# Optimization experiments

Hardware: AMD Instinct MI355X
Metric: run time of the kernel (lower is better)

The kernel has to match this reference:

```python
import jax, jax.numpy as jnp
import numpy as np

N_NODES = 5000
N_STRUCT = 50
PER = N_NODES // N_STRUCT
K = 24
N_EDGES = N_NODES * K
MAX_EDGES = 32
D = 128
HEADS = 4
L = 2
M = 1
NSP = 4
ALL_SPECIES = np.array([1, 6, 7, 8])
R_CUT, R_TRANS = 5.0, 3.0
SPECIES_TABLE = jnp.full((9,), -1, dtype=jnp.int32).at[jnp.asarray(ALL_SPECIES)].set(jnp.arange(NSP, dtype=jnp.int32))

def _ln(x, w, b):
    m = jnp.mean(x, axis=-1, keepdims=True)
    v = jnp.var(x, axis=-1, keepdims=True)
    return (x - m) * jax.lax.rsqrt(v + 1e-5) * w + b

def _block(x, mask, Wq, Wk, Wv, Wo, l1w, l1b, l2w, l2b, W1, b1, W2, b2):
    n, t, d = x.shape
    dh = d // HEADS
    h = _ln(x, l1w, l1b)
    q = (h @ Wq).reshape(n, t, HEADS, dh)
    k = (h @ Wk).reshape(n, t, HEADS, dh)
    v = (h @ Wv).reshape(n, t, HEADS, dh)
    scores = jnp.einsum('nthd,nshd->nhts', q, k) * (1.0 / np.sqrt(dh))
    p = jax.nn.softmax(scores, axis=-1) * mask[:, None, None, :]  # cutoff-weighted keys
    x = x + jnp.einsum('nhts,nshd->nthd', p, v).reshape(n, t, d) @ Wo
    h2 = _ln(x, l2w, l2b)
    return x + jax.nn.gelu(h2 @ W1 + b1) @ W2 + b2

def _transformer(x, mask, params):
    for i in range(L):
        x = _block(x, mask, *(a[i] for a in params))
    return x

def _graph_indices(centers, neighbors):
    e_ids = jnp.arange(N_EDGES, dtype=jnp.int32)
    counts = jnp.zeros((N_NODES,), jnp.int32).at[centers].add(1)
    start = jnp.cumsum(counts) - counts
    slot = e_ids - start[centers]  # centers sorted by construction
    nef_idx = jnp.zeros((N_NODES, MAX_EDGES), jnp.int32).at[centers, slot].set(e_ids)
    nef_mask = jnp.arange(MAX_EDGES, dtype=jnp.int32)[None, :] < counts[:, None]
    keys = centers * N_NODES + neighbors
    order = jnp.argsort(keys)
    corr = order[jnp.searchsorted(keys[order], neighbors * N_NODES + centers)]
    return nef_idx, slot, nef_mask, corr

def _cutoff(r):
    x = (r - R_TRANS) / (R_CUT - R_TRANS)
    smooth = 0.5 * (1.0 + jnp.cos(jnp.pi * x))
    return jnp.where(r < R_TRANS, 1.0, jnp.where(r >= R_CUT, 0.0, smooth))

def _forward(positions, cells, cell_shifts, enc_Wcart, enc_emb_center, enc_emb_neigh, enc_Wcomp, t_Wq, t_Wk, t_Wv, t_Wo, t_ln1w, t_ln1b, t_ln2w, t_ln2b, t_W1, t_b1, t_W2, t_b2, g_contr, g_Wq, g_Wk, g_Wv, g_Wo, g_ln1w, g_ln1b, g_ln2w, g_ln2b, g_W1, g_b1, g_W2, g_b2, readout_W, composition_weights, numbers, centers, neighbors):
    seg = jnp.repeat(jnp.arange(N_STRUCT, dtype=jnp.int32), PER)  # sorted structure ids
    ev = positions[neighbors] - positions[centers] + jnp.einsum('ia,iab->ib', cell_shifts, cells[seg[centers]])
    radial = _cutoff(jnp.sqrt(jnp.sum(ev * ev, axis=-1)))
    elem = SPECIES_TABLE[numbers]
    nef_idx, slot, nef_mask, corr = _graph_indices(centers, neighbors)
    radial_nef = jnp.where(nef_mask, radial[nef_idx], 0.0)
    feats = jnp.concatenate([ev[nef_idx] @ enc_Wcart, enc_emb_center[elem[centers][nef_idx]], enc_emb_neigh[elem[neighbors][nef_idx]]], axis=-1) @ enc_Wcomp
    tparams = (t_Wq, t_Wk, t_Wv, t_Wo, t_ln1w, t_ln1b, t_ln2w, t_ln2b, t_W1, t_b1, t_W2, t_b2)
    feats = _transformer(feats, radial_nef, tparams)
    gparams = (g_Wq, g_Wk, g_Wv, g_Wo, g_ln1w, g_ln1b, g_ln2w, g_ln2b, g_W1, g_b1, g_W2, g_b2)
    for m in range(M):
        new = feats[centers, slot]  # nef -> edge list
        new = jnp.concatenate([new, new[corr]], axis=-1) @ g_contr[m]
        new = _transformer(new[nef_idx], radial_nef, tuple(a[m] for a in gparams))
        feats = feats + new
    ee = (feats @ readout_W)[..., 0] * radial_nef  # [N, MAX_EDGES]
    struct_e = jax.ops.segment_sum(jnp.sum(ee, axis=1), seg, num_segments=N_STRUCT, indices_are_sorted=True)
    comp = jax.ops.segment_sum(jax.nn.one_hot(elem, NSP, dtype=jnp.float32), seg, num_segments=N_STRUCT, indices_are_sorted=True)
    return struct_e + comp @ composition_weights

def setup_inputs():
    key = jax.random.key(0)
    ks = jax.random.split(key, 24)
    deltas = np.concatenate([np.arange(1, K // 2 + 1), -np.arange(1, K // 2 + 1)])
    nb_local = (np.arange(PER)[:, None] + deltas[None, :]) % PER  # symmetric circulant graph per structure
    neighbors = (nb_local[None, :, :] + (np.arange(N_STRUCT) * PER)[:, None, None]).reshape(-1)
    centers = np.repeat(np.arange(N_NODES), K)
    def w(i, shape, s=0.05):
        return (jax.random.normal(ks[i], shape) * s).astype(jnp.float32)
    return {
        'positions': jax.random.normal(ks[0], (N_NODES, 3), dtype=jnp.float32) * 2.0,
        'cells': jnp.tile(jnp.eye(3, dtype=jnp.float32) * 20.0, (N_STRUCT, 1, 1)),
        'cell_shifts': jnp.zeros((N_EDGES, 3), dtype=jnp.float32),
        'enc_Wcart': w(2, (3, D), 0.5),
        'enc_emb_center': w(3, (NSP, D), 1.0),
        'enc_emb_neigh': w(4, (NSP, D), 1.0),
        'enc_Wcomp': w(5, (3 * D, D)),
        't_Wq': w(6, (L, D, D)), 't_Wk': w(7, (L, D, D)), 't_Wv': w(8, (L, D, D)), 't_Wo': w(9, (L, D, D)),
        't_ln1w': jnp.ones((L, D), jnp.float32), 't_ln1b': jnp.zeros((L, D), jnp.float32),
        't_ln2w': jnp.ones((L, D), jnp.float32), 't_ln2b': jnp.zeros((L, D), jnp.float32),
        't_W1': w(10, (L, D, 4 * D)), 't_b1': jnp.zeros((L, 4 * D), jnp.float32),
        't_W2': w(11, (L, 4 * D, D)), 't_b2': jnp.zeros((L, D), jnp.float32),
        'g_contr': w(12, (M, 2 * D, D)),
        'g_Wq': w(13, (M, L, D, D)), 'g_Wk': w(14, (M, L, D, D)), 'g_Wv': w(15, (M, L, D, D)), 'g_Wo': w(16, (M, L, D, D)),
        'g_ln1w': jnp.ones((M, L, D), jnp.float32), 'g_ln1b': jnp.zeros((M, L, D), jnp.float32),
        'g_ln2w': jnp.ones((M, L, D), jnp.float32), 'g_ln2b': jnp.zeros((M, L, D), jnp.float32),
        'g_W1': w(17, (M, L, D, 4 * D)), 'g_b1': jnp.zeros((M, L, 4 * D), jnp.float32),
        'g_W2': w(18, (M, L, 4 * D, D)), 'g_b2': jnp.zeros((M, L, D), jnp.float32),
        'readout_W': w(19, (D, 1)),
        'composition_weights': w(20, (NSP,), 1.0),
        'numbers': jnp.asarray(ALL_SPECIES, dtype=jnp.int32)[jax.random.randint(ks[1], (N_NODES,), 0, NSP)],
        'centers': jnp.asarray(centers, dtype=jnp.int32),
        'neighbors': jnp.asarray(neighbors, dtype=jnp.int32),
    }

def reference(positions, cells, cell_shifts, enc_Wcart, enc_emb_center, enc_emb_neigh, enc_Wcomp, t_Wq, t_Wk, t_Wv, t_Wo, t_ln1w, t_ln1b, t_ln2w, t_ln2b, t_W1, t_b1, t_W2, t_b2, g_contr, g_Wq, g_Wk, g_Wv, g_Wo, g_ln1w, g_ln1b, g_ln2w, g_ln2b, g_W1, g_b1, g_W2, g_b2, readout_W, composition_weights, numbers, centers, neighbors):
    return _forward(positions, cells, cell_shifts, enc_Wcart, enc_emb_center, enc_emb_neigh, enc_Wcomp, t_Wq, t_Wk, t_Wv, t_Wo, t_ln1w, t_ln1b, t_ln2w, t_ln2b, t_W1, t_b1, t_W2, t_b2, g_contr, g_Wq, g_Wk, g_Wv, g_Wo, g_ln1w, g_ln1b, g_ln2w, g_ln2b, g_W1, g_b1, g_W2, g_b2, readout_W, composition_weights, numbers, centers, neighbors)
```

## Files before the change

kernel.cpp:

```cpp
#include <hip/hip_runtime.h>
#include <hip/hip_bf16.h>
#include <math.h>

#define N_NODES 5000
#define N_STRUCT 50
#define PER 100
#define K_NB 24
#define N_EDGES (N_NODES*K_NB)
#define TMAX 32
#define D 128
#define FF 512
#define NTOK (N_NODES*TMAX)

typedef short bf16x8 __attribute__((ext_vector_type(8)));
typedef float f32x4  __attribute__((ext_vector_type(4)));
#define MFMA_B16(a,b,c) __builtin_amdgcn_mfma_f32_16x16x32_bf16(a,b,c,0,0,0)

__device__ __forceinline__ short f2bf(float x){
    return (short)((__float_as_uint(x) + 0x8000u) >> 16);
}
__device__ __forceinline__ short f2bf_rn(float x){
    unsigned u = __float_as_uint(x);
    return (short)((u + 0x7FFFu + ((u>>16)&1u)) >> 16);
}

__device__ __forceinline__ float gelu_f(float x){
    float arg = x * fmaf(x*x, -0.07135481627f, -1.5957691216057308f);
    return x * __builtin_amdgcn_rcpf(1.f + __expf(arg));
}

__device__ __forceinline__ float cutoff_f(float r){
    if (r < 3.f) return 1.f;
    if (r >= 5.f) return 0.f;
    float x = (r-3.f)*0.5f;
    return 0.5f*(1.f + cosf(3.14159265358979323846f * x));
}

__global__ void k_setup(const float* tWq, const float* tWk, const float* tWv, const float* tWo,
                        const float* tW1, const float* tW2, const float* gWq, const float* gWk,
                        const float* gWv, const float* gWo, const float* gW1, const float* gW2,
                        const float* gct, short* __restrict__ WT,
                        const float* __restrict__ pos, const float* __restrict__ cells,
                        const float* __restrict__ shifts, const int* __restrict__ centers,
                        const int* __restrict__ neighbors, float* __restrict__ EV,
                        float* __restrict__ RAD, int* __restrict__ CORR,
                        const int* __restrict__ numbers, int* __restrict__ ELEM,
                        const float* __restrict__ Wcart, const float* __restrict__ embc,
                        const float* __restrict__ embn, const float* __restrict__ Wcomp,
                        float* __restrict__ W3, float* __restrict__ ECn, float* __restrict__ ENn,
                        float* __restrict__ out){
    int b = blockIdx.x, tid = threadIdx.x;
    if (b < 3200){
        const int  sel[25]  = {0,0,1,1,2,2,3,3,4,4,5,5,6,6,7,7,8,8,9,9,10,10,11,11,12};
        const int  lin[25]  = {7,7,7,7,7,7,7,7,7,7,9,9,7,7,7,7,7,7,7,7,7,7,9,9,8};
        const int  lout[25] = {7,7,7,7,7,7,7,7,9,9,7,7,7,7,7,7,7,7,7,7,9,9,7,7,7};
        const int  soff[25] = {0,16384,0,16384,0,16384,0,16384,0,65536,0,65536,
                               0,16384,0,16384,0,16384,0,16384,0,65536,0,65536,0};
        const int  doff[25] = {0,16384,32768,49152,65536,81920,98304,114688,
                               131072,196608,262144,327680,
                               393216,409600,425984,442368,458752,475136,491520,507904,
                               524288,589824,655360,720896,786432};
        int gid = b*256 + tid;
        int r = 0, base = 0;
        while (true){
            int sz = 1 << (lin[r]+lout[r]);
            if (gid < base + sz) break;
            base += sz; r++;
        }
        int d = gid - base;
        int j = d >> lin[r], i = d & ((1<<lin[r])-1);
        const float* src;
        switch (sel[r]){
            case 0: src=tWq; break; case 1: src=tWk; break; case 2: src=tWv; break; case 3: src=tWo; break;
            case 4: src=tW1; break; case 5: src=tW2; break;
            case 6: src=gWq; break; case 7: src=gWk; break; case 8: src=gWv; break; case 9: src=gWo; break;
            case 10: src=gW1; break; case 11: src=gW2; break; default: src=gct; break;
        }
        float v = src[soff[r] + (i<<lout[r]) + j];
        if (sel[r] == 0 || sel[r] == 6) v *= 0.17677669529663689f;
        WT[doff[r] + d] = f2bf_rn(v);
    } else if (b < 3669){
        int e = (b-3200)*256 + tid;
        if (e >= N_EDGES) return;
        int c = centers[e], nb = neighbors[e];
        int st = c / PER;
        const float* cell = cells + st*9;
        float s0 = shifts[e*3+0], s1 = shifts[e*3+1], s2 = shifts[e*3+2];
        float ex = pos[nb*3+0]-pos[c*3+0] + s0*cell[0]+s1*cell[3]+s2*cell[6];
        float ey = pos[nb*3+1]-pos[c*3+1] + s0*cell[1]+s1*cell[4]+s2*cell[7];
        float ez = pos[nb*3+2]-pos[c*3+2] + s0*cell[2]+s1*cell[5]+s2*cell[8];
        EV[e*3+0] = ex; EV[e*3+1] = ey; EV[e*3+2] = ez;
        RAD[e] = cutoff_f(sqrtf(ex*ex+ey*ey+ez*ez));
        int base2 = nb*K_NB, corr = base2;
        for (int k2 = 0; k2 < K_NB; k2++){
            if (neighbors[base2+k2] == c){ corr = base2+k2; break; }
        }
        CORR[e] = corr;
    } else if (b < 3689){
        int i = (b-3669)*256 + tid;
        if (i < N_NODES){
            int z = numbers[i];
            ELEM[i] = (z==1)?0:(z==6)?1:(z==7)?2:(z==8)?3:-1;
        }
    } else if (b == 3689){
        if (tid >= 128) return;
        int j = tid;
        for (int a = 0; a < 3; a++){
            float s = 0;
            for (int i = 0; i < 128; i++) s += Wcart[a*128+i]*Wcomp[i*128+j];
            W3[a*128+j] = s;
        }
        for (int sp = 0; sp < 4; sp++){
            float s1 = 0, s2 = 0;
            for (int i = 0; i < 128; i++){
                s1 += embc[sp*128+i]*Wcomp[(128+i)*128+j];
                s2 += embn[sp*128+i]*Wcomp[(256+i)*128+j];
            }
            ECn[sp*128+j] = s1; ENn[sp*128+j] = s2;
        }
    } else {
        if (tid < N_STRUCT) out[tid] = 0.f;
    }
}

__global__ __launch_bounds__(256) void k_encode(const float* __restrict__ EV,
                         const float* __restrict__ RAD,
                         const int* __restrict__ centers, const int* __restrict__ neighbors,
                         const int* __restrict__ ELEM, const float* __restrict__ W3,
                         const float* __restrict__ ECn, const float* __restrict__ ENn,
                         float* __restrict__ X, float* __restrict__ RADN){
    int n = blockIdx.x, tid = threadIdx.x;
    int s = tid >> 3, l8 = tid & 7;
    int e = (s < K_NB) ? (n*K_NB + s) : 0;
    int ec = ELEM[centers[e]], en = ELEM[neighbors[e]];
    float ev0 = EV[e*3+0], ev1 = EV[e*3+1], ev2 = EV[e*3+2];
    size_t ro = (size_t)(n*32 + s)*128;
    #pragma unroll
    for (int c = 0; c < 4; c++){
        int j = l8*16 + c*4;
        f32x4 wa = *(const f32x4*)&W3[j];
        f32x4 wb = *(const f32x4*)&W3[128+j];
        f32x4 wc = *(const f32x4*)&W3[256+j];
        f32x4 ea = *(const f32x4*)&ECn[ec*128+j];
        f32x4 na = *(const f32x4*)&ENn[en*128+j];
        f32x4 o;
        #pragma unroll
        for (int k = 0; k < 4; k++) o[k] = ev0*wa[k] + ev1*wb[k] + ev2*wc[k] + ea[k] + na[k];
        *(f32x4*)&X[ro + j] = o;
    }
    if (tid < 32) RADN[(size_t)n*32 + tid] = (tid < K_NB) ? RAD[n*K_NB + tid] : 0.f;
}

__global__ __launch_bounds__(256, 2) void k_attn_p(float* __restrict__ X,
        const short* __restrict__ Wqt, const short* __restrict__ Wkt,
        const short* __restrict__ Wvt, const short* __restrict__ Wot,
        const float* __restrict__ lnw, const float* __restrict__ lnb,
        const float* __restrict__ radn){
    __shared__ short hh[32*136];
    __shared__ short Qs[32*136];
    __shared__ short Ks[32*136];
    __shared__ short VT[128*40];
    __shared__ short Ps[4*32*40];
    __shared__ float radl[32];
    const int tid = threadIdx.x, lane = tid & 63, w = tid >> 6;
    const int quad = lane >> 4, l16 = lane & 15;

    bf16x8 wQ[8], wK[8], wV[8], wO[8];
    #pragma unroll
    for (int mt = 0; mt < 2; mt++)
        #pragma unroll
        for (int kk = 0; kk < 4; kk++){
            int ro = (w*32 + mt*16 + l16)*128 + kk*32 + quad*8;
            wQ[mt*4+kk] = *(const bf16x8*)&Wqt[ro];
            wK[mt*4+kk] = *(const bf16x8*)&Wkt[ro];
            wV[mt*4+kk] = *(const bf16x8*)&Wvt[ro];
            wO[mt*4+kk] = *(const bf16x8*)&Wot[ro];
        }

    for (int node = blockIdx.x; node < N_NODES; node += 768){
        float* Xn = X + (size_t)node*4096;
        {
            int row = tid >> 3, l8 = tid & 7;
            f32x4 v[4];
            #pragma unroll
            for (int c = 0; c < 4; c++) v[c] = *(const f32x4*)&Xn[row*128 + l8*16 + c*4];
            float s = 0, ss = 0;
            #pragma unroll
            for (int c = 0; c < 4; c++){
                #pragma unroll
                for (int k = 0; k < 4; k++){ s += v[c][k]; ss += v[c][k]*v[c][k]; }
            }
            #pragma unroll
            for (int m = 1; m < 8; m <<= 1){ s += __shfl_xor(s, m); ss += __shfl_xor(ss, m); }
            float mean = s*(1.f/128.f);
            float rstd = rsqrtf(ss*(1.f/128.f) - mean*mean + 1e-5f);
            #pragma unroll
            for (int c = 0; c < 4; c++){
                f32x4 wv4 = *(const f32x4*)&lnw[l8*16 + c*4];
                f32x4 bv4 = *(const f32x4*)&lnb[l8*16 + c*4];
                short4 pk;
                pk.x = f2bf((v[c][0]-mean)*rstd*wv4[0] + bv4[0]);
                pk.y = f2bf((v[c][1]-mean)*rstd*wv4[1] + bv4[1]);
                pk.z = f2bf((v[c][2]-mean)*rstd*wv4[2] + bv4[2]);
                pk.w = f2bf((v[c][3]-mean)*rstd*wv4[3] + bv4[3]);
                *(short4*)&hh[row*136 + l8*16 + c*4] = pk;
            }
        }
        if (tid < 32) radl[tid] = radn[(size_t)node*32 + tid];
        __syncthreads();

        {
            f32x4 z = {0.f,0.f,0.f,0.f};
            f32x4 qacc[4] = {z,z,z,z}, kacc[4] = {z,z,z,z};
            #pragma unroll
            for (int kk = 0; kk < 4; kk++){
                bf16x8 h0 = *(const bf16x8*)&hh[(l16)*136    + kk*32 + quad*8];
                bf16x8 h1 = *(const bf16x8*)&hh[(16+l16)*136 + kk*32 + quad*8];
                #pragma unroll
                for (int mt = 0; mt < 2; mt++){
                    qacc[mt*2+0] = MFMA_B16(wQ[mt*4+kk], h0, qacc[mt*2+0]);
                    qacc[mt*2+1] = MFMA_B16(wQ[mt*4+kk], h1, qacc[mt*2+1]);
                    kacc[mt*2+0] = MFMA_B16(wK[mt*4+kk], h0, kacc[mt*2+0]);
                    kacc[mt*2+1] = MFMA_B16(wK[mt*4+kk], h1, kacc[mt*2+1]);
                }
            }
            #pragma unroll
            for (int mt = 0; mt < 2; mt++){
                #pragma unroll
                for (int nt = 0; nt < 2; nt++){
                    int t = nt*16 + l16, jb = w*32 + mt*16 + quad*4;
                    short4 pk;
                    pk.x = f2bf(qacc[mt*2+nt][0]); pk.y = f2bf(qacc[mt*2+nt][1]);
                    pk.z = f2bf(qacc[mt*2+nt][2]); pk.w = f2bf(qacc[mt*2+nt][3]);
                    *(short4*)&Qs[t*136 + jb] = pk;
                    short4 pk2;
                    pk2.x = f2bf(kacc[mt*2+nt][0]); pk2.y = f2bf(kacc[mt*2+nt][1]);
                    pk2.z = f2bf(kacc[mt*2+nt][2]); pk2.w = f2bf(kacc[mt*2+nt][3]);
                    *(short4*)&Ks[t*136 + jb] = pk2;
                }
            }
        }
        {
            f32x4 z = {0.f,0.f,0.f,0.f};
            f32x4 vacc[4] = {z,z,z,z};
            #pragma unroll
            for (int kk = 0; kk < 4; kk++){
                bf16x8 h0 = *(const bf16x8*)&hh[(l16)*136    + kk*32 + quad*8];
                bf16x8 h1 = *(const bf16x8*)&hh[(16+l16)*136 + kk*32 + quad*8];
                #pragma unroll
                for (int mt = 0; mt < 2; mt++){
                    vacc[0*2+mt] = MFMA_B16(h0, wV[mt*4+kk], vacc[0*2+mt]);
                    vacc[1*2+mt] = MFMA_B16(h1, wV[mt*4+kk], vacc[1*2+mt]);
                }
            }
            #pragma unroll
            for (int mt = 0; mt < 2; mt++){
                #pragma unroll
                for (int nt = 0; nt < 2; nt++){
                    int j = w*32 + nt*16 + l16, sb = mt*16 + quad*4;
                    f32x4 r4 = *(const f32x4*)&radl[sb];
                    short4 pk;
                    pk.x = f2bf(vacc[mt*2+nt][0]*r4[0]); pk.y = f2bf(vacc[mt*2+nt][1]*r4[1]);
                    pk.z = f2bf(vacc[mt*2+nt][2]*r4[2]); pk.w = f2bf(vacc[mt*2+nt][3]*r4[3]);
                    *(short4*)&VT[j*40 + sb] = pk;
                }
            }
        }
        {
            const int h = w;
            bf16x8 qa0 = *(const bf16x8*)&Qs[(l16)*136    + h*32 + quad*8];
            bf16x8 qa1 = *(const bf16x8*)&Qs[(16+l16)*136 + h*32 + quad*8];
            bf16x8 kb0 = *(const bf16x8*)&Ks[(l16)*136    + h*32 + quad*8];
            bf16x8 kb1 = *(const bf16x8*)&Ks[(16+l16)*136 + h*32 + quad*8];
            f32x4 z = {0.f,0.f,0.f,0.f};
            f32x4 sc00 = MFMA_B16(qa0, kb0, z), sc01 = MFMA_B16(qa0, kb1, z);
            f32x4 sc10 = MFMA_B16(qa1, kb0, z), sc11 = MFMA_B16(qa1, kb1, z);
            #pragma unroll
            for (int mt = 0; mt < 2; mt++){
                f32x4 s0 = mt ? sc10 : sc00, s1 = mt ? sc11 : sc01;
                #pragma unroll
                for (int r = 0; r < 4; r++){
                    float mx = fmaxf(s0[r], s1[r]);
                    #pragma unroll
                    for (int dlt = 1; dlt < 16; dlt <<= 1) mx = fmaxf(mx, __shfl_xor(mx, dlt));
                    float e0 = __expf(s0[r]-mx), e1 = __expf(s1[r]-mx);
                    float sm = e0 + e1;
                    #pragma unroll
                    for (int dlt = 1; dlt < 16; dlt <<= 1) sm += __shfl_xor(sm, dlt);
                    float inv = __builtin_amdgcn_rcpf(sm);
                    int t = mt*16 + quad*4 + r;
                    Ps[h*1280 + t*40 + l16]      = f2bf(e0*inv);
                    Ps[h*1280 + t*40 + 16 + l16] = f2bf(e1*inv);
                }
            }
        }
        short* OB = Qs;
        {
            const int h = w;
            bf16x8 pa0 = *(const bf16x8*)&Ps[h*1280 + (l16)*40    + quad*8];
            bf16x8 pa1 = *(const bf16x8*)&Ps[h*1280 + (16+l16)*40 + quad*8];
            bf16x8 vb0 = *(const bf16x8*)&VT[(h*32 + l16)*40      + quad*8];
            bf16x8 vb1 = *(const bf16x8*)&VT[(h*32 + 16 + l16)*40 + quad*8];
            f32x4 z = {0.f,0.f,0.f,0.f};
            f32x4 o00 = MFMA_B16(pa0, vb0, z), o01 = MFMA_B16(pa0, vb1, z);
            f32x4 o10 = MFMA_B16(pa1, vb0, z), o11 = MFMA_B16(pa1, vb1, z);
            #pragma unroll
            for (int mt = 0; mt < 2; mt++){
                #pragma unroll
                for (int nt = 0; nt < 2; nt++){
                    f32x4 ov = mt ? (nt ? o11 : o10) : (nt ? o01 : o00);
                    int j = w*32 + nt*16 + l16;
                    #pragma unroll
                    for (int r = 0; r < 4; r++){
                        int t = mt*16 + quad*4 + r;
                        OB[t*136 + j] = f2bf(ov[r]);
                    }
                }
            }
        }
        __syncthreads();
        {
            f32x4 z = {0.f,0.f,0.f,0.f};
            f32x4 oc[4] = {z,z,z,z};
            #pragma unroll
            for (int kk = 0; kk < 4; kk++){
                bf16x8 a0 = *(const bf16x8*)&OB[(l16)*136    + kk*32 + quad*8];
                bf16x8 a1 = *(const bf16x8*)&OB[(16+l16)*136 + kk*32 + quad*8];
                #pragma unroll
                for (int nt = 0; nt < 2; nt++){
                    oc[0+nt] = MFMA_B16(a0, wO[nt*4+kk], oc[0+nt]);
                    oc[2+nt] = MFMA_B16(a1, wO[nt*4+kk], oc[2+nt]);
                }
            }
            #pragma unroll
            for (int mt = 0; mt < 2; mt++){
                #pragma unroll
                for (int nt = 0; nt < 2; nt++){
                    int j2 = w*32 + nt*16 + l16;
                    #pragma unroll
                    for (int r = 0; r < 4; r++){
                        int t = mt*16 + quad*4 + r;
                        Xn[t*128 + j2] += oc[mt*2+nt][r];
                    }
                }
            }
        }
    }
}

__global__ __launch_bounds__(512, 2) void k_ffn_p(float* __restrict__ X,
        const short* __restrict__ W1t, const short* __restrict__ W2t,
        const float* __restrict__ B1, const float* __restrict__ B2,
        const float* __restrict__ lnw, const float* __restrict__ lnb){
    __shared__ float xs[32*132];
    __shared__ short hh[32*136];
    __shared__ short mid[32*520];
    const int tid = threadIdx.x, lane = tid & 63, w = tid >> 6;
    const int quad = lane >> 4, l16 = lane & 15;

    bf16x8 wA[16];
    #pragma unroll
    for (int mt = 0; mt < 4; mt++)
        #pragma unroll
        for (int kk = 0; kk < 4; kk++)
            wA[mt*4+kk] = *(const bf16x8*)&W1t[(size_t)(w*64+mt*16+l16)*128 + kk*32 + quad*8];
    bf16x8 wB[16];
    #pragma unroll
    for (int kk = 0; kk < 16; kk++)
        wB[kk] = *(const bf16x8*)&W2t[(size_t)(w*16+l16)*512 + kk*32 + quad*8];
    f32x4 bb1[4];
    #pragma unroll
    for (int mt = 0; mt < 4; mt++) bb1[mt] = *(const f32x4*)&B1[w*64 + mt*16 + quad*4];
    const float b2v = B2[w*16 + l16];

    for (int tile = blockIdx.x; tile < NTOK/32; tile += 512){
        float* Xg = X + (size_t)tile*4096;
        {
            int row = tid >> 4, lc = tid & 15;
            f32x4 v0 = *(const f32x4*)&Xg[row*128 + lc*8];
            f32x4 v1 = *(const f32x4*)&Xg[row*128 + lc*8 + 4];
            *(f32x4*)&xs[row*132 + lc*8]     = v0;
            *(f32x4*)&xs[row*132 + lc*8 + 4] = v1;
            float s = 0, ss = 0;
            #pragma unroll
            for (int k = 0; k < 4; k++){ s += v0[k]+v1[k]; ss += v0[k]*v0[k]+v1[k]*v1[k]; }
            #pragma unroll
            for (int m = 1; m < 16; m <<= 1){ s += __shfl_xor(s, m); ss += __shfl_xor(ss, m); }
            float mean = s*(1.f/128.f);
            float rstd = rsqrtf(ss*(1.f/128.f) - mean*mean + 1e-5f);
            f32x4 w0 = *(const f32x4*)&lnw[lc*8], w1 = *(const f32x4*)&lnw[lc*8+4];
            f32x4 g0 = *(const f32x4*)&lnb[lc*8], g1 = *(const f32x4*)&lnb[lc*8+4];
            short4 pa, pb;
            pa.x = f2bf((v0[0]-mean)*rstd*w0[0] + g0[0]);
            pa.y = f2bf((v0[1]-mean)*rstd*w0[1] + g0[1]);
            pa.z = f2bf((v0[2]-mean)*rstd*w0[2] + g0[2]);
            pa.w = f2bf((v0[3]-mean)*rstd*w0[3] + g0[3]);
            pb.x = f2bf((v1[0]-mean)*rstd*w1[0] + g1[0]);
            pb.y = f2bf((v1[1]-mean)*rstd*w1[1] + g1[1]);
            pb.z = f2bf((v1[2]-mean)*rstd*w1[2] + g1[2]);
            pb.w = f2bf((v1[3]-mean)*rstd*w1[3] + g1[3]);
            *(short4*)&hh[row*136 + lc*8]     = pa;
            *(short4*)&hh[row*136 + lc*8 + 4] = pb;
        }
        __syncthreads();
        {
            f32x4 z = {0.f,0.f,0.f,0.f};
            f32x4 acc[8];
            #pragma unroll
            for (int i = 0; i < 8; i++) acc[i] = z;
            #pragma unroll
            for (int kk = 0; kk < 4; kk++){
                bf16x8 h0 = *(const bf16x8*)&hh[(l16)*136    + kk*32 + quad*8];
                bf16x8 h1 = *(const bf16x8*)&hh[(16+l16)*136 + kk*32 + quad*8];
                #pragma unroll
                for (int mt = 0; mt < 4; mt++){
                    acc[mt*2+0] = MFMA_B16(wA[mt*4+kk], h0, acc[mt*2+0]);
                    acc[mt*2+1] = MFMA_B16(wA[mt*4+kk], h1, acc[mt*2+1]);
                }
            }
            #pragma unroll
            for (int mt = 0; mt < 4; mt++){
                int fb = w*64 + mt*16 + quad*4;
                #pragma unroll
                for (int nt = 0; nt < 2; nt++){
                    int t = nt*16 + l16;
                    short4 pk;
                    pk.x = f2bf(gelu_f(acc[mt*2+nt][0] + bb1[mt][0]));
                    pk.y = f2bf(gelu_f(acc[mt*2+nt][1] + bb1[mt][1]));
                    pk.z = f2bf(gelu_f(acc[mt*2+nt][2] + bb1[mt][2]));
                    pk.w = f2bf(gelu_f(acc[mt*2+nt][3] + bb1[mt][3]));
                    *(short4*)&mid[t*520 + fb] = pk;
                }
            }
        }
        __syncthreads();
        {
            f32x4 z = {0.f,0.f,0.f,0.f};
            f32x4 o0 = z, o1 = z;
            #pragma unroll
            for (int kk = 0; kk < 16; kk++){
                bf16x8 a0 = *(const bf16x8*)&mid[(l16)*520    + kk*32 + quad*8];
                bf16x8 a1 = *(const bf16x8*)&mid[(16+l16)*520 + kk*32 + quad*8];
                o0 = MFMA_B16(a0, wB[kk], o0);
                o1 = MFMA_B16(a1, wB[kk], o1);
            }
            int j = w*16 + l16;
            #pragma unroll
            for (int r = 0; r < 4; r++){
                int t0 = quad*4 + r, t1 = 16 + quad*4 + r;
                Xg[t0*128 + j] = xs[t0*132 + j] + o0[r] + b2v;
                Xg[t1*128 + j] = xs[t1*132 + j] + o1[r] + b2v;
            }
        }
        __syncthreads();
    }
}

__global__ __launch_bounds__(256) void k_contract_mfma(const float* __restrict__ X,
        const int* __restrict__ centers, const int* __restrict__ CORR,
        const short* __restrict__ gct, float* __restrict__ Y){
    __shared__ short ab[32*264];
    const int tid = threadIdx.x, lane = tid & 63, w = tid >> 6;
    const int quad = lane >> 4, l16 = lane & 15;
    const int e0 = blockIdx.x*32;
    for (int idx = tid; idx < 2048; idx += 256){
        int r = idx >> 6, c4 = idx & 63;
        int e = e0 + r, srcRow;
        if (c4 < 32){ int c = centers[e]; srcRow = c*32 + (e - c*K_NB); }
        else        { int ec = CORR[e]; int c = centers[ec]; srcRow = c*32 + (ec - c*K_NB); }
        float4 v = *(const float4*)&X[(size_t)srcRow*128 + (c4 & 31)*4];
        short4 pk; pk.x = f2bf(v.x); pk.y = f2bf(v.y); pk.z = f2bf(v.z); pk.w = f2bf(v.w);
        *(short4*)&ab[r*264 + c4*4] = pk;
    }
    __syncthreads();
    f32x4 z = {0.f,0.f,0.f,0.f};
    f32x4 o[4] = {z,z,z,z};
    #pragma unroll
    for (int kk = 0; kk < 8; kk++){
        bf16x8 a0 = *(const bf16x8*)&ab[(l16)*264    + kk*32 + quad*8];
        bf16x8 a1 = *(const bf16x8*)&ab[(16+l16)*264 + kk*32 + quad*8];
        #pragma unroll
        for (int nt = 0; nt < 2; nt++){
            bf16x8 bw = *(const bf16x8*)&gct[(size_t)(w*32+nt*16+l16)*256 + kk*32 + quad*8];
            o[0+nt] = MFMA_B16(a0, bw, o[0+nt]);
            o[2+nt] = MFMA_B16(a1, bw, o[2+nt]);
        }
    }
    #pragma unroll
    for (int mt = 0; mt < 2; mt++){
        #pragma unroll
        for (int nt = 0; nt < 2; nt++){
            int j = w*32 + nt*16 + l16;
            #pragma unroll
            for (int r = 0; r < 4; r++){
                int e = e0 + mt*16 + quad*4 + r;
                int c = e / K_NB, slot = e - c*K_NB;
                Y[((size_t)c*32 + slot)*128 + j] = o[mt*2+nt][r];
            }
        }
    }
}

__global__ void k_padfill(float* __restrict__ Y){
    int idx = blockIdx.x*256 + threadIdx.x;
    if (idx >= N_NODES*8*D) return;
    int j = idx & 127, rs = idx >> 7;
    int n = rs >> 3, sr = rs & 7;
    Y[((size_t)n*32 + K_NB + sr)*D + j] = Y[j];
}

__global__ __launch_bounds__(256) void k_readout(const float* __restrict__ X,
        const float* __restrict__ Y, const float* __restrict__ rW,
        const float* __restrict__ radn, const int* __restrict__ ELEM,
        const float* __restrict__ cw, float* __restrict__ out){
    __shared__ float rws[128];
    __shared__ float wsum[4];
    int S = blockIdx.x >> 3, sub = blockIdx.x & 7;
    int tid = threadIdx.x, lane = tid & 63, wv = tid >> 6;
    if (tid < 128) rws[tid] = rW[tid];
    __syncthreads();
    float acc = 0.f;
    for (int r = sub*400 + wv; r < (sub+1)*400; r += 4){
        size_t row = (size_t)S*PER*32 + r;
        float rad = radn[row];
        if (rad != 0.f){
            const float* xr = X + row*D;
            const float* yr = Y + row*D;
            acc += rad * ((xr[lane]+yr[lane])*rws[lane] + (xr[lane+64]+yr[lane+64])*rws[lane+64]);
        }
    }
    if (sub == 0){
        for (int nl = tid; nl < PER; nl += 256) acc += cw[ELEM[S*PER + nl]];
    }
    #pragma unroll
    for (int m = 1; m < 64; m <<= 1) acc += __shfl_xor(acc, m);
    if (lane == 0) wsum[wv] = acc;
    __syncthreads();
    if (tid == 0) atomicAdd(&out[S], wsum[0]+wsum[1]+wsum[2]+wsum[3]);
}

extern "C" void kernel_launch(void* const* d_in, const int* in_sizes, int n_in,
                              void* d_out, int out_size, void* d_ws, size_t ws_size,
                              hipStream_t stream){
    const float* positions   = (const float*)d_in[0];
    const float* cells       = (const float*)d_in[1];
    const float* cell_shifts = (const float*)d_in[2];
    const float* enc_Wcart   = (const float*)d_in[3];
    const float* enc_emb_c   = (const float*)d_in[4];
    const float* enc_emb_n   = (const float*)d_in[5];
    const float* enc_Wcomp   = (const float*)d_in[6];
    const float* t_Wq  = (const float*)d_in[7];
    const float* t_Wk  = (const float*)d_in[8];
    const float* t_Wv  = (const float*)d_in[9];
    const float* t_Wo  = (const float*)d_in[10];
    const float* t_ln1w = (const float*)d_in[11];
    const float* t_ln1b = (const float*)d_in[12];
    const float* t_ln2w = (const float*)d_in[13];
    const float* t_ln2b = (const float*)d_in[14];
    const float* t_W1  = (const float*)d_in[15];
    const float* t_b1  = (const float*)d_in[16];
    const float* t_W2  = (const float*)d_in[17];
    const float* t_b2  = (const float*)d_in[18];
    const float* g_contr = (const float*)d_in[19];
    const float* g_Wq  = (const float*)d_in[20];
    const float* g_Wk  = (const float*)d_in[21];
    const float* g_Wv  = (const float*)d_in[22];
    const float* g_Wo  = (const float*)d_in[23];
    const float* g_ln1w = (const float*)d_in[24];
    const float* g_ln1b = (const float*)d_in[25];
    const float* g_ln2w = (const float*)d_in[26];
    const float* g_ln2b = (const float*)d_in[27];
    const float* g_W1  = (const float*)d_in[28];
    const float* g_b1  = (const float*)d_in[29];
    const float* g_W2  = (const float*)d_in[30];
    const float* g_b2  = (const float*)d_in[31];
    const float* readout_W = (const float*)d_in[32];
    const float* comp_w    = (const float*)d_in[33];
    const int* numbers   = (const int*)d_in[34];
    const int* centers   = (const int*)d_in[35];
    const int* neighbors = (const int*)d_in[36];

    float* ws = (float*)d_ws;
    float* X    = ws;
    float* Y    = X + (size_t)NTOK*D;
    float* EV   = Y + (size_t)NTOK*D;
    float* RAD  = EV + (size_t)N_EDGES*3;
    float* RADN = RAD + N_EDGES;
    float* W3   = RADN + NTOK;
    float* ECn  = W3 + 3*128;
    float* ENn  = ECn + 4*128;
    int*   ELEM = (int*)(ENn + 4*128);
    int*   CORR = ELEM + N_NODES;
    short* WT   = (short*)(CORR + N_EDGES);

    const short *tWqt = WT,           *tWkt = WT + 32768, *tWvt = WT + 65536, *tWot = WT + 98304;
    const short *tW1t = WT + 131072,  *tW2t = WT + 262144;
    const short *gWqt = WT + 393216,  *gWkt = WT + 425984, *gWvt = WT + 458752, *gWot = WT + 491520;
    const short *gW1t = WT + 524288,  *gW2t = WT + 655360, *gctT = WT + 786432;

    k_setup<<<3691, 256, 0, stream>>>(t_Wq, t_Wk, t_Wv, t_Wo, t_W1, t_W2,
                                      g_Wq, g_Wk, g_Wv, g_Wo, g_W1, g_W2, g_contr, WT,
                                      positions, cells, cell_shifts, centers, neighbors,
                                      EV, RAD, CORR, numbers, ELEM,
                                      enc_Wcart, enc_emb_c, enc_emb_n, enc_Wcomp,
                                      W3, ECn, ENn, (float*)d_out);
    k_encode<<<N_NODES, 256, 0, stream>>>(EV, RAD, centers, neighbors, ELEM, W3, ECn, ENn, X, RADN);

    for (int l = 0; l < 2; l++){
        k_attn_p<<<768, 256, 0, stream>>>(X, tWqt + l*16384, tWkt + l*16384,
                                          tWvt + l*16384, tWot + l*16384,
                                          t_ln1w + l*128, t_ln1b + l*128, RADN);
        k_ffn_p<<<512, 512, 0, stream>>>(X, tW1t + l*65536, tW2t + l*65536,
                                         t_b1 + l*512, t_b2 + l*128,
                                         t_ln2w + l*128, t_ln2b + l*128);
    }

    k_contract_mfma<<<N_EDGES/32, 256, 0, stream>>>(X, centers, CORR, gctT, Y);
    k_padfill<<<(N_NODES*8*D+255)/256, 256, 0, stream>>>(Y);

    for (int l = 0; l < 2; l++){
        k_attn_p<<<768, 256, 0, stream>>>(Y, gWqt + l*16384, gWkt + l*16384,
                                          gWvt + l*16384, gWot + l*16384,
                                          g_ln1w + l*128, g_ln1b + l*128, RADN);
        k_ffn_p<<<512, 512, 0, stream>>>(Y, gW1t + l*65536, gW2t + l*65536,
                                         g_b1 + l*512, g_b2 + l*128,
                                         g_ln2w + l*128, g_ln2b + l*128);
    }

    k_readout<<<N_STRUCT*8, 256, 0, stream>>>(X, Y, readout_W, RADN, ELEM, comp_w, (float*)d_out);
}
```

Baseline: 1.072 ms.

## Fuse readout into final FFN epilogue and composition sum into setup

The separate readout kernel is removed. The last graph-transformer FFN launch now computes the cutoff-weighted dot product of (X+Y) with the readout weights directly from its output registers, reduces it per block and atomically adds it to the structure energy. The composition-weight sum moves into the setup kernel. This avoids writing Y and then re-reading both X and Y in a separate launch, at the cost of an extra X read, an extra block barrier and an atomic in the FFN epilogue. The final Y values are no longer stored.

```diff
diff --git a/kernel.cpp b/kernel.cpp
--- a/kernel.cpp
+++ b/kernel.cpp
@@ -48,7 +48,7 @@
                         const float* __restrict__ Wcart, const float* __restrict__ embc,
                         const float* __restrict__ embn, const float* __restrict__ Wcomp,
                         float* __restrict__ W3, float* __restrict__ ECn, float* __restrict__ ENn,
-                        float* __restrict__ out){
+                        const float* __restrict__ cw, float* __restrict__ out){
     int b = blockIdx.x, tid = threadIdx.x;
     if (b < 3200){
         const int  sel[25]  = {0,0,1,1,2,2,3,3,4,4,5,5,6,6,7,7,8,8,9,9,10,10,11,11,12};
@@ -119,7 +119,15 @@
             ECn[sp*128+j] = s1; ENn[sp*128+j] = s2;
         }
     } else {
-        if (tid < N_STRUCT) out[tid] = 0.f;
+        if (tid < N_STRUCT){
+            float s = 0.f;
+            for (int nl = 0; nl < PER; nl++){
+                int z = numbers[tid*PER + nl];
+                int el = (z==1)?0:(z==6)?1:(z==7)?2:3;
+                s += cw[el];
+            }
+            out[tid] = s;
+        }
     }
 }
 
@@ -351,10 +359,14 @@
 __global__ __launch_bounds__(512, 2) void k_ffn_p(float* __restrict__ X,
         const short* __restrict__ W1t, const short* __restrict__ W2t,
         const float* __restrict__ B1, const float* __restrict__ B2,
-        const float* __restrict__ lnw, const float* __restrict__ lnb){
+        const float* __restrict__ lnw, const float* __restrict__ lnb,
+        const float* __restrict__ rW, const float* __restrict__ Xo,
+        const float* __restrict__ radn, float* __restrict__ out){
     __shared__ float xs[32*132];
     __shared__ short hh[32*136];
     __shared__ short mid[32*520];
+    __shared__ float radl2[32];
+    __shared__ float wsumR[8];
     const int tid = threadIdx.x, lane = tid & 63, w = tid >> 6;
     const int quad = lane >> 4, l16 = lane & 15;
 
@@ -372,6 +384,7 @@
     #pragma unroll
     for (int mt = 0; mt < 4; mt++) bb1[mt] = *(const f32x4*)&B1[w*64 + mt*16 + quad*4];
     const float b2v = B2[w*16 + l16];
+    const float rwv = rW ? rW[w*16 + l16] : 0.f;
 
     for (int tile = blockIdx.x; tile < NTOK/32; tile += 512){
         float* Xg = X + (size_t)tile*4096;
@@ -402,6 +415,7 @@
             *(short4*)&hh[row*136 + lc*8]     = pa;
             *(short4*)&hh[row*136 + lc*8 + 4] = pb;
         }
+        if (rW && tid < 32) radl2[tid] = radn[(size_t)tile*32 + tid];
         __syncthreads();
         {
             f32x4 z = {0.f,0.f,0.f,0.f};
@@ -445,14 +459,37 @@
                 o1 = MFMA_B16(a1, wB[kk], o1);
             }
             int j = w*16 + l16;
-            #pragma unroll
-            for (int r = 0; r < 4; r++){
-                int t0 = quad*4 + r, t1 = 16 + quad*4 + r;
-                Xg[t0*128 + j] = xs[t0*132 + j] + o0[r] + b2v;
-                Xg[t1*128 + j] = xs[t1*132 + j] + o1[r] + b2v;
+            if (!rW){
+                #pragma unroll
+                for (int r = 0; r < 4; r++){
+                    int t0 = quad*4 + r, t1 = 16 + quad*4 + r;
+                    Xg[t0*128 + j] = xs[t0*132 + j] + o0[r] + b2v;
+                    Xg[t1*128 + j] = xs[t1*132 + j] + o1[r] + b2v;
+                }
+            } else {
+                const float* Xon = Xo + (size_t)tile*4096;
+                float part = 0.f;
+                #pragma unroll
+                for (int r = 0; r < 4; r++){
+                    int t0 = quad*4 + r, t1 = 16 + quad*4 + r;
+                    float y0 = xs[t0*132 + j] + o0[r] + b2v;
+                    float y1 = xs[t1*132 + j] + o1[r] + b2v;
+                    part += (Xon[t0*128 + j] + y0) * radl2[t0];
+                    part += (Xon[t1*128 + j] + y1) * radl2[t1];
+                }
+                part *= rwv;
+                #pragma unroll
+                for (int m = 1; m < 64; m <<= 1) part += __shfl_xor(part, m);
+                if (lane == 0) wsumR[w] = part;
             }
         }
         __syncthreads();
+        if (rW && tid == 0){
+            float tot = 0.f;
+            #pragma unroll
+            for (int i = 0; i < 8; i++) tot += wsumR[i];
+            atomicAdd(&out[tile/PER], tot);
+        }
     }
 }
 
@@ -507,36 +544,6 @@
     int j = idx & 127, rs = idx >> 7;
     int n = rs >> 3, sr = rs & 7;
     Y[((size_t)n*32 + K_NB + sr)*D + j] = Y[j];
-}
-
-__global__ __launch_bounds__(256) void k_readout(const float* __restrict__ X,
-        const float* __restrict__ Y, const float* __restrict__ rW,
-        const float* __restrict__ radn, const int* __restrict__ ELEM,
-        const float* __restrict__ cw, float* __restrict__ out){
-    __shared__ float rws[128];
-    __shared__ float wsum[4];
-    int S = blockIdx.x >> 3, sub = blockIdx.x & 7;
-    int tid = threadIdx.x, lane = tid & 63, wv = tid >> 6;
-    if (tid < 128) rws[tid] = rW[tid];
-    __syncthreads();
-    float acc = 0.f;
-    for (int r = sub*400 + wv; r < (sub+1)*400; r += 4){
-        size_t row = (size_t)S*PER*32 + r;
-        float rad = radn[row];
-        if (rad != 0.f){
-            const float* xr = X + row*D;
-            const float* yr = Y + row*D;
-            acc += rad * ((xr[lane]+yr[lane])*rws[lane] + (xr[lane+64]+yr[lane+64])*rws[lane+64]);
-        }
-    }
-    if (sub == 0){
-        for (int nl = tid; nl < PER; nl += 256) acc += cw[ELEM[S*PER + nl]];
-    }
-    #pragma unroll
-    for (int m = 1; m < 64; m <<= 1) acc += __shfl_xor(acc, m);
-    if (lane == 0) wsum[wv] = acc;
-    __syncthreads();
-    if (tid == 0) atomicAdd(&out[S], wsum[0]+wsum[1]+wsum[2]+wsum[3]);
 }
 
 extern "C" void kernel_launch(void* const* d_in, const int* in_sizes, int n_in,
@@ -603,7 +610,7 @@
                                       positions, cells, cell_shifts, centers, neighbors,
                                       EV, RAD, CORR, numbers, ELEM,
                                       enc_Wcart, enc_emb_c, enc_emb_n, enc_Wcomp,
-                                      W3, ECn, ENn, (float*)d_out);
+                                      W3, ECn, ENn, comp_w, (float*)d_out);
     k_encode<<<N_NODES, 256, 0, stream>>>(EV, RAD, centers, neighbors, ELEM, W3, ECn, ENn, X, RADN);
 
     for (int l = 0; l < 2; l++){
@@ -612,7 +619,8 @@
                                           t_ln1w + l*128, t_ln1b + l*128, RADN);
         k_ffn_p<<<512, 512, 0, stream>>>(X, tW1t + l*65536, tW2t + l*65536,
                                          t_b1 + l*512, t_b2 + l*128,
-                                         t_ln2w + l*128, t_ln2b + l*128);
+                                         t_ln2w + l*128, t_ln2b + l*128,
+                                         nullptr, nullptr, nullptr, nullptr);
     }
 
     k_contract_mfma<<<N_EDGES/32, 256, 0, stream>>>(X, centers, CORR, gctT, Y);
@@ -624,8 +632,10 @@
                                           g_ln1w + l*128, g_ln1b + l*128, RADN);
         k_ffn_p<<<512, 512, 0, stream>>>(Y, gW1t + l*65536, gW2t + l*65536,
                                          g_b1 + l*512, g_b2 + l*128,
-                                         g_ln2w + l*128, g_ln2b + l*128);
-    }
-
-    k_readout<<<N_STRUCT*8, 256, 0, stream>>>(X, Y, readout_W, RADN, ELEM, comp_w, (float*)d_out);
-}
+                                         g_ln2w + l*128, g_ln2b + l*128,
+                                         (l == 1) ? readout_W : nullptr,
+                                         (l == 1) ? X : nullptr,
+                                         (l == 1) ? RADN : nullptr,
+                                         (l == 1) ? (float*)d_out : nullptr);
+    }
+}
```

After: 1.062 ms. No clear change (-0.9%).
